# Kernel optimization log

Measured on AMD Instinct MI355X. Metric: run time of the kernel, lower is better.

Reference implementation:

```python
import jax, jax.numpy as jnp
import numpy as np
import math

HEADS, IN_DIM, OUT_DIM, N = 8, 256, 64, 4096

def _glorot(key, shape):
    fan = shape[-2] + shape[-1]
    lim = math.sqrt(6.0 / fan)
    return jax.random.uniform(key, shape, jnp.float32, -lim, lim)

def setup_inputs() -> dict:
    key = jax.random.key(0)
    ks = jax.random.split(key, 6)
    return {
        "input_x": jax.random.normal(ks[0], (N, IN_DIM), jnp.float32),
        "WQ": _glorot(ks[1], (HEADS, IN_DIM, OUT_DIM)),
        "WK": _glorot(ks[2], (HEADS, IN_DIM, OUT_DIM)),
        "WV": _glorot(ks[3], (HEADS, IN_DIM, OUT_DIM)),
        "lin_w": _glorot(ks[4], (OUT_DIM, HEADS * OUT_DIM)),
        "lin_b": jnp.zeros((OUT_DIM,), jnp.float32),
    }

def reference(input_x, WQ, WK, WV, lin_w, lin_b):
    # Q,K,V: [H, N, D] via broadcasted matmul of [N,in] @ [H,in,D]
    Q = jnp.einsum('ni,hid->hnd', input_x, WQ)
    K = jnp.einsum('ni,hid->hnd', input_x, WK)
    V = jnp.einsum('ni,hid->hnd', input_x, WV)
    scores = jnp.einsum('hnd,hmd->hnm', Q, K)  # [H, N, N]
    # Original adds diag_embed(diag(scores) - 1e20): diagonal -> 2*orig - 1e20
    idx = jnp.arange(scores.shape[-1])
    scores = scores.at[:, idx, idx].add(scores[:, idx, idx] - 1e20)
    attn = jax.nn.softmax(scores / math.sqrt(OUT_DIM), axis=-1)
    attn_x = jnp.einsum('hnm,hmd->hnd', attn, V)  # [H, N, D]
    # cat heads along feature dim: [N, H*D]
    attn_cat = jnp.transpose(attn_x, (1, 0, 2)).reshape(attn_x.shape[1], -1)
    return attn_cat @ lin_w.T + lin_b
```

## Files before the change

### kernel.cpp

```cpp
#include <hip/hip_runtime.h>
#include <hip/hip_bf16.h>

#define SEQ  4096
#define HEADS 8
#define IND  256
#define OUTD 64
#define NSPLIT 4
#define QBLK 128
#define TILES_PER_SLICE (SEQ / 64 / NSPLIT)

typedef __attribute__((ext_vector_type(8))) short bf16x8;
typedef __attribute__((ext_vector_type(4))) float f32x4;

__device__ __forceinline__ unsigned short f2bf(float f) {
  union { __hip_bfloat16 h; unsigned short u; } c;
  c.h = __float2bfloat16(f);
  return c.u;
}
__device__ __forceinline__ float bf2f(unsigned short u) {
  union { unsigned u; float f; } c;
  c.u = ((unsigned)u) << 16;
  return c.f;
}
__device__ __forceinline__ unsigned pk2(float hi, float lo) {
  return __builtin_amdgcn_perm(__builtin_bit_cast(unsigned, hi),
                               __builtin_bit_cast(unsigned, lo), 0x07060302u);
}
__device__ __forceinline__ int pcol(int k) {
  return (k >> 5) * 32 + ((k >> 2) & 3) * 8 + ((k >> 4) & 1) * 4 + (k & 3);
}

__global__ void prep_kernel(const float* __restrict__ WQ,
                            const float* __restrict__ WK,
                            const float* __restrict__ WV,
                            const float* __restrict__ LW,
                            unsigned short* __restrict__ WTQ,
                            unsigned short* __restrict__ WTK,
                            unsigned short* __restrict__ WTV,
                            unsigned short* __restrict__ LWB) {
  const int NW = HEADS * IND * OUTD;
  const int NL = OUTD * HEADS * OUTD;
  int i = blockIdx.x * 256 + threadIdx.x;
  if (i < 3 * NW) {
    int which = i / NW;
    int r = i % NW;
    int h = r / (IND * OUTD);
    int rem = r % (IND * OUTD);
    int d = rem / IND;
    int ii = rem % IND;
    const float* W = (which == 0) ? WQ : ((which == 1) ? WK : WV);
    float v = W[(h * IND + ii) * OUTD + d];
    if (which == 0) v *= 0.125f * 1.44269504088896f;
    unsigned short* DST = (which == 0) ? WTQ : ((which == 1) ? WTK : WTV);
    DST[h * OUTD * IND + d * IND + ii] = f2bf(v);
  } else if (i < 3 * NW + NL) {
    int k = i - 3 * NW;
    LWB[k] = f2bf(LW[k]);
  }
}

__global__ __launch_bounds__(256) void proj_kernel(
    const float* __restrict__ X,
    const unsigned short* __restrict__ WTQ,
    const unsigned short* __restrict__ WTK,
    const unsigned short* __restrict__ WTV,
    unsigned short* __restrict__ Qo,
    unsigned short* __restrict__ KS,
    unsigned short* __restrict__ VS) {
  const int tb = blockIdx.x;
  const int h  = blockIdx.y;

  __shared__ unsigned short Xl[64 * 72];
  __shared__ unsigned short Wl[3][64 * 72];

  const int tid = threadIdx.x;
  const int lane = tid & 63;
  const int w = tid >> 6;
  const int m16 = lane & 15;
  const int g = lane >> 4;

  const unsigned short* W0 = WTQ + h * OUTD * IND;
  const unsigned short* W1 = WTK + h * OUTD * IND;
  const unsigned short* W2 = WTV + h * OUTD * IND;

  f32x4 acc[3][4];
#pragma unroll
  for (int z = 0; z < 3; ++z)
#pragma unroll
    for (int ns = 0; ns < 4; ++ns) {
      f32x4 z4 = {0.f, 0.f, 0.f, 0.f};
      acc[z][ns] = z4;
    }

  for (int kb = 0; kb < 4; ++kb) {
    if (kb) __syncthreads();
    for (int s = tid; s < 512; s += 256) {
      int row = s >> 3, sg = s & 7;
      const float* xs = X + (size_t)(tb * 64 + row) * IND + kb * 64 + sg * 8;
      float4 x0 = *(const float4*)xs;
      float4 x1 = *(const float4*)(xs + 4);
      uint4 u;
      u.x = ((unsigned)f2bf(x0.y) << 16) | f2bf(x0.x);
      u.y = ((unsigned)f2bf(x0.w) << 16) | f2bf(x0.z);
      u.z = ((unsigned)f2bf(x1.y) << 16) | f2bf(x1.x);
      u.w = ((unsigned)f2bf(x1.w) << 16) | f2bf(x1.z);
      *(uint4*)(&Xl[row * 72 + sg * 8]) = u;
      *(uint4*)(&Wl[0][row * 72 + sg * 8]) =
          *(const uint4*)(W0 + (size_t)row * IND + kb * 64 + sg * 8);
      *(uint4*)(&Wl[1][row * 72 + sg * 8]) =
          *(const uint4*)(W1 + (size_t)row * IND + kb * 64 + sg * 8);
      *(uint4*)(&Wl[2][row * 72 + sg * 8]) =
          *(const uint4*)(W2 + (size_t)row * IND + kb * 64 + sg * 8);
    }
    __syncthreads();
    bf16x8 xa0 = *(const bf16x8*)(&Xl[(w * 16 + m16) * 72 + g * 8]);
    bf16x8 xa1 = *(const bf16x8*)(&Xl[(w * 16 + m16) * 72 + 32 + g * 8]);
#pragma unroll
    for (int z = 0; z < 2; ++z)
#pragma unroll
      for (int ns = 0; ns < 4; ++ns) {
        bf16x8 b0 = *(const bf16x8*)(&Wl[z][(ns * 16 + m16) * 72 + g * 8]);
        bf16x8 b1 = *(const bf16x8*)(&Wl[z][(ns * 16 + m16) * 72 + 32 + g * 8]);
        acc[z][ns] = __builtin_amdgcn_mfma_f32_16x16x32_bf16(xa0, b0, acc[z][ns], 0, 0, 0);
        acc[z][ns] = __builtin_amdgcn_mfma_f32_16x16x32_bf16(xa1, b1, acc[z][ns], 0, 0, 0);
      }
    bf16x8 wa0 = *(const bf16x8*)(&Wl[2][(w * 16 + m16) * 72 + g * 8]);
    bf16x8 wa1 = *(const bf16x8*)(&Wl[2][(w * 16 + m16) * 72 + 32 + g * 8]);
#pragma unroll
    for (int ns = 0; ns < 4; ++ns) {
      bf16x8 b0 = *(const bf16x8*)(&Xl[(ns * 16 + m16) * 72 + g * 8]);
      bf16x8 b1 = *(const bf16x8*)(&Xl[(ns * 16 + m16) * 72 + 32 + g * 8]);
      acc[2][ns] = __builtin_amdgcn_mfma_f32_16x16x32_bf16(wa0, b0, acc[2][ns], 0, 0, 0);
      acc[2][ns] = __builtin_amdgcn_mfma_f32_16x16x32_bf16(wa1, b1, acc[2][ns], 0, 0, 0);
    }
  }
#pragma unroll
  for (int ns = 0; ns < 4; ++ns)
#pragma unroll
    for (int r = 0; r < 4; ++r) {
      int token = tb * 64 + w * 16 + 4 * g + r;
      int d = ns * 16 + m16;
      Qo[(size_t)h * SEQ * OUTD + (size_t)token * OUTD + d] = f2bf(acc[0][ns][r]);
    }
  {
    unsigned short* O = KS + ((size_t)(h * 64 + tb)) * 4096;
#pragma unroll
    for (int ns = 0; ns < 4; ++ns)
#pragma unroll
      for (int r = 0; r < 4; ++r) {
        int rk = w * 16 + 4 * g + r;
        int d = ns * 16 + m16;
        int c = d >> 3;
        int idx = rk * 64 + ((c ^ (rk & 7)) << 3) + (d & 7);
        O[idx] = f2bf(acc[1][ns][r]);
      }
  }
  {
    unsigned short* O = VS + ((size_t)(h * 64 + tb)) * 4096;
#pragma unroll
    for (int ns = 0; ns < 4; ++ns) {
      int cp = pcol(ns * 16 + m16);
      int c = cp >> 3, j = cp & 7;
#pragma unroll
      for (int r = 0; r < 4; ++r) {
        int rv = w * 16 + 4 * g + r;
        int idx = rv * 64 + ((c ^ (rv & 7)) << 3) + j;
        O[idx] = f2bf(acc[2][ns][r]);
      }
    }
  }
}

__global__ __launch_bounds__(256, 4) void attn_kernel(
    const unsigned short* __restrict__ Q,
    const unsigned short* __restrict__ KS,
    const unsigned short* __restrict__ VS,
    unsigned short* __restrict__ PART,
    float* __restrict__ L) {
  const int qb = blockIdx.x;
  const int h  = blockIdx.y;
  const int sl = blockIdx.z;
  const int kb0 = sl * TILES_PER_SLICE;
  const unsigned short* Qh = Q + (size_t)h * SEQ * OUTD;

  __shared__ unsigned short Kl[2][4096];
  __shared__ unsigned short Vl[2][4096];

  const int tid = threadIdx.x;
  const int lane = tid & 63;
  const int w = tid >> 6;
  const int m16 = lane & 15;
  const int g = lane >> 4;
  const int e = m16 & 7;
  const int c0s = ((g ^ e) << 3);
  const int c1s = (((g + 4) ^ e) << 3);

  const int qrowA = qb * QBLK + w * 16 + m16;
  const int qrowB = qrowA + 64;
  bf16x8 qfA0 = *(const bf16x8*)(Qh + (size_t)qrowA * OUTD + g * 8);
  bf16x8 qfA1 = *(const bf16x8*)(Qh + (size_t)qrowA * OUTD + 32 + g * 8);
  bf16x8 qfB0 = *(const bf16x8*)(Qh + (size_t)qrowB * OUTD + g * 8);
  bf16x8 qfB1 = *(const bf16x8*)(Qh + (size_t)qrowB * OUTD + 32 + g * 8);

  f32x4 accA[4], accB[4], acc5A, acc5B;
#pragma unroll
  for (int s4 = 0; s4 < 4; ++s4) {
    f32x4 z4 = {0.f, 0.f, 0.f, 0.f};
    accA[s4] = z4; accB[s4] = z4;
  }
  { f32x4 z4 = {0.f, 0.f, 0.f, 0.f}; acc5A = z4; acc5B = z4; }
  const f32x4 zero4 = {0.f, 0.f, 0.f, 0.f};
  bf16x8 ones;
#pragma unroll
  for (int j = 0; j < 8; ++j) ones[j] = (short)0x3F80;

  const unsigned short* kg = KS + ((size_t)(h * 64 + kb0)) * 4096 + w * 512 + lane * 8;
  const unsigned short* vg = VS + ((size_t)(h * 64 + kb0)) * 4096 + w * 512 + lane * 8;

  auto stage = [&](int buf) {
    __builtin_amdgcn_global_load_lds(kg, &Kl[buf][w * 512], 16, 0, 0);
    __builtin_amdgcn_global_load_lds(kg + 2048, &Kl[buf][2048 + w * 512], 16, 0, 0);
    __builtin_amdgcn_global_load_lds(vg, &Vl[buf][w * 512], 16, 0, 0);
    __builtin_amdgcn_global_load_lds(vg + 2048, &Vl[buf][2048 + w * 512], 16, 0, 0);
    kg += 4096; vg += 4096;
  };

  stage(0);
  __syncthreads();

  for (int it = 0; it < TILES_PER_SLICE; ++it) {
    const int kb = kb0 + it;
    const int cur = it & 1;
    if (it < TILES_PER_SLICE - 1) stage(cur ^ 1);

    f32x4 stA[4], stB[4];
    __builtin_amdgcn_s_setprio(1);
#pragma unroll
    for (int t = 0; t < 4; ++t) {
      const unsigned short* krow = &Kl[cur][(t * 16 + m16) * 64];
      bf16x8 ka0 = *(const bf16x8*)(krow + c0s);
      bf16x8 ka1 = *(const bf16x8*)(krow + c1s);
      stA[t] = __builtin_amdgcn_mfma_f32_16x16x32_bf16(ka0, qfA0, zero4, 0, 0, 0);
      stA[t] = __builtin_amdgcn_mfma_f32_16x16x32_bf16(ka1, qfA1, stA[t], 0, 0, 0);
      stB[t] = __builtin_amdgcn_mfma_f32_16x16x32_bf16(ka0, qfB0, zero4, 0, 0, 0);
      stB[t] = __builtin_amdgcn_mfma_f32_16x16x32_bf16(ka1, qfB1, stB[t], 0, 0, 0);
    }
    __builtin_amdgcn_s_setprio(0);

    if (kb == 2 * qb) {
#pragma unroll
      for (int t = 0; t < 4; ++t)
#pragma unroll
        for (int r = 0; r < 4; ++r)
          if (t == w && (4 * g + r) == m16) stA[t][r] = -1e30f;
    }
    if (kb == 2 * qb + 1) {
#pragma unroll
      for (int t = 0; t < 4; ++t)
#pragma unroll
        for (int r = 0; r < 4; ++r)
          if (t == w && (4 * g + r) == m16) stB[t][r] = -1e30f;
    }

    float eA[16], eB[16];
#pragma unroll
    for (int t = 0; t < 4; ++t)
#pragma unroll
      for (int r = 0; r < 4; ++r) {
        eA[t * 4 + r] = exp2f(stA[t][r]);
        eB[t * 4 + r] = exp2f(stB[t][r]);
      }
    uint4 uA0, uA1, uB0, uB1;
    uA0.x = pk2(eA[1], eA[0]);   uA0.y = pk2(eA[3], eA[2]);
    uA0.z = pk2(eA[5], eA[4]);   uA0.w = pk2(eA[7], eA[6]);
    uA1.x = pk2(eA[9], eA[8]);   uA1.y = pk2(eA[11], eA[10]);
    uA1.z = pk2(eA[13], eA[12]); uA1.w = pk2(eA[15], eA[14]);
    uB0.x = pk2(eB[1], eB[0]);   uB0.y = pk2(eB[3], eB[2]);
    uB0.z = pk2(eB[5], eB[4]);   uB0.w = pk2(eB[7], eB[6]);
    uB1.x = pk2(eB[9], eB[8]);   uB1.y = pk2(eB[11], eB[10]);
    uB1.z = pk2(eB[13], eB[12]); uB1.w = pk2(eB[15], eB[14]);
    bf16x8 pbA0 = __builtin_bit_cast(bf16x8, uA0);
    bf16x8 pbA1 = __builtin_bit_cast(bf16x8, uA1);
    bf16x8 pbB0 = __builtin_bit_cast(bf16x8, uB0);
    bf16x8 pbB1 = __builtin_bit_cast(bf16x8, uB1);

    __builtin_amdgcn_s_setprio(1);
#pragma unroll
    for (int s4 = 0; s4 < 4; ++s4) {
      const unsigned short* vrow = &Vl[cur][(s4 * 16 + m16) * 64];
      bf16x8 va0 = *(const bf16x8*)(vrow + c0s);
      bf16x8 va1 = *(const bf16x8*)(vrow + c1s);
      accA[s4] = __builtin_amdgcn_mfma_f32_16x16x32_bf16(va0, pbA0, accA[s4], 0, 0, 0);
      accA[s4] = __builtin_amdgcn_mfma_f32_16x16x32_bf16(va1, pbA1, accA[s4], 0, 0, 0);
      accB[s4] = __builtin_amdgcn_mfma_f32_16x16x32_bf16(va0, pbB0, accB[s4], 0, 0, 0);
      accB[s4] = __builtin_amdgcn_mfma_f32_16x16x32_bf16(va1, pbB1, accB[s4], 0, 0, 0);
    }
    acc5A = __builtin_amdgcn_mfma_f32_16x16x32_bf16(ones, pbA0, acc5A, 0, 0, 0);
    acc5A = __builtin_amdgcn_mfma_f32_16x16x32_bf16(ones, pbA1, acc5A, 0, 0, 0);
    acc5B = __builtin_amdgcn_mfma_f32_16x16x32_bf16(ones, pbB0, acc5B, 0, 0, 0);
    acc5B = __builtin_amdgcn_mfma_f32_16x16x32_bf16(ones, pbB1, acc5B, 0, 0, 0);
    __builtin_amdgcn_s_setprio(0);

    __syncthreads();
  }

  const size_t baseA = (((size_t)sl * HEADS + h) * SEQ + qrowA) * OUTD;
  const size_t baseB = (((size_t)sl * HEADS + h) * SEQ + qrowB) * OUTD;
#pragma unroll
  for (int s4 = 0; s4 < 4; ++s4) {
    uint2 pkA, pkB;
    pkA.x = pk2(accA[s4][1], accA[s4][0]);
    pkA.y = pk2(accA[s4][3], accA[s4][2]);
    pkB.x = pk2(accB[s4][1], accB[s4][0]);
    pkB.y = pk2(accB[s4][3], accB[s4][2]);
    *(uint2*)(&PART[baseA + s4 * 16 + 4 * g]) = pkA;
    *(uint2*)(&PART[baseB + s4 * 16 + 4 * g]) = pkB;
  }
  if (g == 0) {
    L[((size_t)sl * HEADS + h) * SEQ + qrowA] = acc5A[0];
    L[((size_t)sl * HEADS + h) * SEQ + qrowB] = acc5B[0];
  }
}

__global__ __launch_bounds__(128) void final_kernel(
    const unsigned short* __restrict__ PART, const float* __restrict__ L,
    const unsigned short* __restrict__ LWB, const float* __restrict__ LB,
    float* __restrict__ OUT) {
  __shared__ float Rl[64 * 20];
  const int q0 = blockIdx.x * 16;
  const int tid = threadIdx.x;
  const int wv = tid >> 6, lane = tid & 63;
  const int m16 = lane & 15, g = lane >> 4;

  f32x4 acc[4];
#pragma unroll
  for (int ns = 0; ns < 4; ++ns) { f32x4 z4 = {0.f, 0.f, 0.f, 0.f}; acc[ns] = z4; }

#pragma unroll
  for (int kbi = 0; kbi < 4; ++kbi) {
    const int kb = wv * 4 + kbi;
    float lsum = 0.f;
#pragma unroll
    for (int s2 = 0; s2 < NSPLIT; ++s2)
      lsum += L[((size_t)s2 * HEADS + kb) * SEQ + q0 + m16];
    float inv = 1.f / lsum;
    float va[8], vb[8];
#pragma unroll
    for (int j = 0; j < 8; ++j) { va[j] = 0.f; vb[j] = 0.f; }
#pragma unroll
    for (int s2 = 0; s2 < NSPLIT; ++s2) {
      const unsigned short* p =
          PART + (((size_t)s2 * HEADS + kb) * SEQ + q0 + m16) * OUTD;
      bf16x8 t0 = *(const bf16x8*)(p + g * 8);
      bf16x8 t1 = *(const bf16x8*)(p + 32 + g * 8);
#pragma unroll
      for (int j = 0; j < 8; ++j) {
        va[j] += bf2f((unsigned short)t0[j]);
        vb[j] += bf2f((unsigned short)t1[j]);
      }
    }
    uint4 u0, u1;
    u0.x = pk2(va[1] * inv, va[0] * inv); u0.y = pk2(va[3] * inv, va[2] * inv);
    u0.z = pk2(va[5] * inv, va[4] * inv); u0.w = pk2(va[7] * inv, va[6] * inv);
    u1.x = pk2(vb[1] * inv, vb[0] * inv); u1.y = pk2(vb[3] * inv, vb[2] * inv);
    u1.z = pk2(vb[5] * inv, vb[4] * inv); u1.w = pk2(vb[7] * inv, vb[6] * inv);
    bf16x8 a0 = __builtin_bit_cast(bf16x8, u0);
    bf16x8 a1 = __builtin_bit_cast(bf16x8, u1);
#pragma unroll
    for (int ns = 0; ns < 4; ++ns) {
      const unsigned short* lw = LWB + (size_t)(ns * 16 + m16) * 512 + kb * 64;
      bf16x8 b0 = *(const bf16x8*)(lw + g * 8);
      bf16x8 b1 = *(const bf16x8*)(lw + 32 + g * 8);
      acc[ns] = __builtin_amdgcn_mfma_f32_16x16x32_bf16(a0, b0, acc[ns], 0, 0, 0);
      acc[ns] = __builtin_amdgcn_mfma_f32_16x16x32_bf16(a1, b1, acc[ns], 0, 0, 0);
    }
  }

  if (wv == 1) {
#pragma unroll
    for (int ns = 0; ns < 4; ++ns)
      *(f32x4*)(&Rl[lane * 20 + ns * 4]) = acc[ns];
  }
  __syncthreads();
  if (wv == 0) {
#pragma unroll
    for (int ns = 0; ns < 4; ++ns) {
      f32x4 o = acc[ns] + *(const f32x4*)(&Rl[lane * 20 + ns * 4]);
      float b = LB[ns * 16 + m16];
#pragma unroll
      for (int r = 0; r < 4; ++r)
        OUT[(size_t)(q0 + 4 * g + r) * OUTD + ns * 16 + m16] = o[r] + b;
    }
  }
}

extern "C" void kernel_launch(void* const* d_in, const int* in_sizes, int n_in,
                              void* d_out, int out_size, void* d_ws, size_t ws_size,
                              hipStream_t stream) {
  const float* X  = (const float*)d_in[0];
  const float* WQ = (const float*)d_in[1];
  const float* WK = (const float*)d_in[2];
  const float* WV = (const float*)d_in[3];
  const float* LW = (const float*)d_in[4];
  const float* LB = (const float*)d_in[5];

  char* ws = (char*)d_ws;
  unsigned short* Qb  = (unsigned short*)ws;
  unsigned short* KS  = Qb + (size_t)HEADS * SEQ * OUTD;
  unsigned short* VS  = KS + (size_t)HEADS * SEQ * OUTD;
  unsigned short* LWB = VS + (size_t)HEADS * SEQ * OUTD;
  char* region2 = (char*)(LWB + (size_t)OUTD * HEADS * OUTD);

  unsigned short* WTQ = (unsigned short*)region2;
  unsigned short* WTK = WTQ + (size_t)HEADS * OUTD * IND;
  unsigned short* WTV = WTK + (size_t)HEADS * OUTD * IND;

  unsigned short* PART = (unsigned short*)region2;
  float* Lml = (float*)(region2 + (size_t)NSPLIT * HEADS * SEQ * OUTD * 2);

  const int total_prep = 3 * HEADS * IND * OUTD + OUTD * HEADS * OUTD;
  prep_kernel<<<(total_prep + 255) / 256, 256, 0, stream>>>(
      WQ, WK, WV, LW, WTQ, WTK, WTV, LWB);
  proj_kernel<<<dim3(64, 8), 256, 0, stream>>>(X, WTQ, WTK, WTV, Qb, KS, VS);
  attn_kernel<<<dim3(SEQ / QBLK, 8, NSPLIT), 256, 0, stream>>>(Qb, KS, VS, PART, Lml);
  final_kernel<<<256, 128, 0, stream>>>(PART, Lml, LWB, LB, (float*)d_out);
}
```

Before: 79.41 us.

## Triple-buffer K/V tiles with partial vmcnt waits and use raw exp2

Moves the K/V LDS staging from double to triple buffering, prefetching two tiles ahead. The full __syncthreads is replaced by an explicit s_waitcnt vmcnt(4) plus s_barrier, so loads for the next tile can stay in flight while the current tile is computed. exp2f is swapped for the hardware v_exp_f32 intrinsic, and the tile loop is fully unrolled. Occupancy drops from 4 to 3 blocks per CU because of the extra 16KB of LDS, and the hand-written vmcnt counts depend on every stage issuing exactly four loads.

```diff
diff --git a/kernel.cpp b/kernel.cpp
--- a/kernel.cpp
+++ b/kernel.cpp
@@ -21,6 +21,15 @@
   union { unsigned u; float f; } c;
   c.u = ((unsigned)u) << 16;
   return c.f;
+}
+__device__ __forceinline__ float fast_exp2(float x) {
+#if __has_builtin(__builtin_amdgcn_exp2f)
+  return __builtin_amdgcn_exp2f(x);
+#else
+  float r;
+  asm("v_exp_f32 %0, %1" : "=v"(r) : "v"(x));
+  return r;
+#endif
 }
 __device__ __forceinline__ unsigned pk2(float hi, float lo) {
   return __builtin_amdgcn_perm(__builtin_bit_cast(unsigned, hi),
@@ -171,7 +180,7 @@
   }
 }
 
-__global__ __launch_bounds__(256, 4) void attn_kernel(
+__global__ __launch_bounds__(256, 3) void attn_kernel(
     const unsigned short* __restrict__ Q,
     const unsigned short* __restrict__ KS,
     const unsigned short* __restrict__ VS,
@@ -183,8 +192,8 @@
   const int kb0 = sl * TILES_PER_SLICE;
   const unsigned short* Qh = Q + (size_t)h * SEQ * OUTD;
 
-  __shared__ unsigned short Kl[2][4096];
-  __shared__ unsigned short Vl[2][4096];
+  __shared__ unsigned short Kl[3][4096];
+  __shared__ unsigned short Vl[3][4096];
 
   const int tid = threadIdx.x;
   const int lane = tid & 63;
@@ -226,12 +235,16 @@
   };
 
   stage(0);
-  __syncthreads();
-
+  stage(1);
+  asm volatile("s_waitcnt vmcnt(4)" ::: "memory");
+  __builtin_amdgcn_s_barrier();
+  asm volatile("" ::: "memory");
+
+#pragma unroll
   for (int it = 0; it < TILES_PER_SLICE; ++it) {
     const int kb = kb0 + it;
-    const int cur = it & 1;
-    if (it < TILES_PER_SLICE - 1) stage(cur ^ 1);
+    const int cur = it % 3;
+    if (it + 2 < TILES_PER_SLICE) stage((it + 2) % 3);
 
     f32x4 stA[4], stB[4];
     __builtin_amdgcn_s_setprio(1);
@@ -267,8 +280,8 @@
     for (int t = 0; t < 4; ++t)
 #pragma unroll
       for (int r = 0; r < 4; ++r) {
-        eA[t * 4 + r] = exp2f(stA[t][r]);
-        eB[t * 4 + r] = exp2f(stB[t][r]);
+        eA[t * 4 + r] = fast_exp2(stA[t][r]);
+        eB[t * 4 + r] = fast_exp2(stB[t][r]);
       }
     uint4 uA0, uA1, uB0, uB1;
     uA0.x = pk2(eA[1], eA[0]);   uA0.y = pk2(eA[3], eA[2]);
@@ -301,7 +314,15 @@
     acc5B = __builtin_amdgcn_mfma_f32_16x16x32_bf16(ones, pbB1, acc5B, 0, 0, 0);
     __builtin_amdgcn_s_setprio(0);
 
-    __syncthreads();
+    if (it < TILES_PER_SLICE - 1) {
+      if (it < TILES_PER_SLICE - 2) {
+        asm volatile("s_waitcnt vmcnt(4)" ::: "memory");
+      } else {
+        asm volatile("s_waitcnt vmcnt(0)" ::: "memory");
+      }
+      __builtin_amdgcn_s_barrier();
+      asm volatile("" ::: "memory");
+    }
   }
 
   const size_t baseA = (((size_t)sl * HEADS + h) * SEQ + qrowA) * OUTD;
```

Measured after the change: 68.12 us. 1.17x faster.
